# Kernel tuning notes

Hardware: AMD Instinct MI355X
Metric: run time of the kernel (lower is better)

## Reference

```python
import jax, jax.numpy as jnp
import numpy as np

N, B, S, A, H, E = 8, 8192, 64, 16, 512, 4  # agents, batch, state, action, hidden, heads
D = H // E  # attend_dim


def setup_inputs() -> dict:
    key = jax.random.key(0)
    ks = jax.random.split(key, 12)
    g = lambda k, shape, fan: (jax.random.normal(k, shape, jnp.float32) / np.float32(np.sqrt(fan)))
    return {
        "states": jax.random.normal(ks[0], (N, B, S), jnp.float32),
        "actions": jax.random.normal(ks[1], (N, B, A), jnp.float32),
        # per-agent state encoder (Linear + LeakyReLU)
        "Ws": g(ks[2], (N, S, H), S), "bs": jnp.zeros((N, H), jnp.float32),
        # per-agent state-action encoder
        "Wsa": g(ks[3], (N, S + A, H), S + A), "bsa": jnp.zeros((N, H), jnp.float32),
        # shared per-head extractors (key/selector bias-free, value has bias+LeakyReLU)
        "Wk": g(ks[4], (E, H, D), H),
        "Wsel": g(ks[5], (E, H, D), H),
        "Wv": g(ks[6], (E, H, D), H), "bv": jnp.zeros((E, D), jnp.float32),
        # per-agent critic head (2H -> H -> 1)
        "Wc1": g(ks[7], (N, 2 * H, H), 2 * H), "bc1": jnp.zeros((N, H), jnp.float32),
        "Wc2": g(ks[8], (N, H, 1), H), "bc2": jnp.zeros((N, 1), jnp.float32),
        # per-agent value head (2H -> H -> 1)
        "Wv1": g(ks[9], (N, 2 * H, H), 2 * H), "bv1": jnp.zeros((N, H), jnp.float32),
        "Wv2": g(ks[10], (N, H, 1), H), "bv2": jnp.zeros((N, 1), jnp.float32),
    }


def reference(states, actions, Ws, bs, Wsa, bsa, Wk, Wsel, Wv, bv,
              Wc1, bc1, Wc2, bc2, Wv1, bv1, Wv2, bv2):
    lrelu = jax.nn.leaky_relu  # slope 0.01, matches nn.LeakyReLU default
    # encoders: [N,B,H]
    s_enc = lrelu(jnp.einsum('nbs,nsh->nbh', states, Ws) + bs[:, None, :])
    sa = jnp.concatenate([states, actions], axis=-1)
    sa_enc = lrelu(jnp.einsum('nbi,nih->nbh', sa, Wsa) + bsa[:, None, :])
    # per-head keys/selectors/values: [B,E,N,D]
    keys = jnp.einsum('nbh,ehd->bend', sa_enc, Wk)
    sels = jnp.einsum('nbh,ehd->bend', sa_enc, Wsel)
    vals = lrelu(jnp.einsum('nbh,ehd->bend', sa_enc, Wv) + bv[None, :, None, :])
    # each agent i attends over all agents j (including itself; no mask in source)
    logits = jnp.einsum('beid,bejd->beij', sels, keys) / jnp.float32(np.sqrt(D))
    weights = jax.nn.softmax(logits, axis=-1)
    other = jnp.einsum('beij,bejd->beid', weights, vals)  # [B,E,N,D]
    other = jnp.transpose(other, (2, 0, 1, 3)).reshape(N, B, H)  # heads concat -> [N,B,H]
    critic_in = jnp.concatenate([sa_enc, other], axis=-1)  # [N,B,2H]
    value_in = jnp.concatenate([s_enc, other], axis=-1)
    q = jnp.einsum('nbh,nho->nbo', lrelu(jnp.einsum('nbi,nih->nbh', critic_in, Wc1) + bc1[:, None, :]), Wc2) + bc2[:, None, :]
    v = jnp.einsum('nbh,nho->nbo', lrelu(jnp.einsum('nbi,nih->nbh', value_in, Wv1) + bv1[:, None, :]), Wv2) + bv2[:, None, :]
    return q, v  # each [N,B,1]
```

## Files before the change

### kernel.cpp

```cpp
#include <hip/hip_runtime.h>


#define DEVI __device__ __forceinline__

typedef unsigned short us16;
typedef __bf16 bf16x8 __attribute__((ext_vector_type(8)));
typedef float f32x4 __attribute__((ext_vector_type(4)));
typedef unsigned short u16x8 __attribute__((ext_vector_type(8)));

DEVI us16 f2bf(float f) {
  unsigned u = __builtin_bit_cast(unsigned, f);
  u += 0x7FFFu + ((u >> 16) & 1u);
  return (us16)(u >> 16);
}
DEVI float bf2f(us16 h) {
  unsigned u = ((unsigned)h) << 16;
  return __builtin_bit_cast(float, u);
}
DEVI float lrelu(float v) { return v > 0.f ? v : 0.01f * v; }
DEVI int pk2(float a, float b) { return (int)f2bf(a) | ((int)f2bf(b) << 16); }

DEVI void gload16(const us16* g, us16* l) {
  __builtin_amdgcn_global_load_lds(
      (const __attribute__((address_space(1))) void*)g,
      (__attribute__((address_space(3))) void*)l, 16, 0, 0);
}

__global__ void tconvSA_k(const float* __restrict__ wsrc, const float* __restrict__ wsasrc,
                          us16* __restrict__ wst, us16* __restrict__ wsat)
{
  __shared__ float t[32][33];
  const int zz = blockIdx.z;
  const int m = zz >> 3, s = zz & 7;
  const int K = m ? 80 : 64, Kpad = m ? 96 : 64;
  const float* src = m ? (wsasrc + (long)s * 80 * 512) : (wsrc + (long)s * 64 * 512);
  us16* dst = m ? (wsat + (long)s * 512 * 96) : (wst + (long)s * 512 * 64);
  const int k0 = blockIdx.x * 32, o0 = blockIdx.y * 32;
  const int lx = threadIdx.x, ly = threadIdx.y;
#pragma unroll
  for (int i = 0; i < 4; i++) {
    int k = k0 + ly + i * 8, o = o0 + lx;
    float v = 0.f;
    if (k < K) v = src[(long)k * 512 + o];
    t[ly + i * 8][lx] = v;
  }
  __syncthreads();
#pragma unroll
  for (int i = 0; i < 4; i++) {
    int o = o0 + ly + i * 8, k = k0 + lx;
    if (k < Kpad)
      dst[(long)o * Kpad + k] = f2bf(t[lx][ly + i * 8]);
  }
}

__global__ void tconv3_k(const float* __restrict__ wk, const float* __restrict__ wsel,
                         const float* __restrict__ wv, us16* __restrict__ dst)
{
  __shared__ float t[32][33];
  const int zz = blockIdx.z;
  const int e = zz & 3, m = zz >> 2;
  const float* src = ((m == 0) ? wk : (m == 1) ? wsel : wv) + (long)e * 512 * 128;
  us16* d = dst + (long)e * 384 * 512 + (long)(m * 128) * 512;
  const int k0 = blockIdx.x * 32, o0 = blockIdx.y * 32;
  const int lx = threadIdx.x, ly = threadIdx.y;
#pragma unroll
  for (int i = 0; i < 4; i++)
    t[ly + i * 8][lx] = src[(long)(k0 + ly + i * 8) * 128 + (o0 + lx)];
  __syncthreads();
#pragma unroll
  for (int i = 0; i < 4; i++)
    d[(long)(o0 + ly + i * 8) * 512 + (k0 + lx)] = f2bf(t[lx][ly + i * 8]);
}

__global__ void tconvC_k(const float* __restrict__ c1, const float* __restrict__ v1,
                         us16* __restrict__ dc, us16* __restrict__ dv)
{
  __shared__ float t[32][33];
  const int zz = blockIdx.z;
  const int n = zz & 7, m = zz >> 3;
  const float* src = ((m == 0) ? c1 : v1) + (long)n * 1024 * 512;
  us16* dst = ((m == 0) ? dc : dv) + (long)n * 512 * 1024;
  const int k0 = blockIdx.x * 32, o0 = blockIdx.y * 32;
  const int lx = threadIdx.x, ly = threadIdx.y;
#pragma unroll
  for (int i = 0; i < 4; i++)
    t[ly + i * 8][lx] = src[(long)(k0 + ly + i * 8) * 512 + (o0 + lx)];
  __syncthreads();
#pragma unroll
  for (int i = 0; i < 4; i++)
    dst[(long)(o0 + ly + i * 8) * 1024 + (k0 + lx)] = f2bf(t[lx][ly + i * 8]);
}

enum { ASRC_F32 = 2, ASRC_F32_CAT = 3 };

template <int ASRC, int KTOT>
__global__ __launch_bounds__(256, 4)
void enc_gemm_k(const float* __restrict__ Ap, long aSlice,
                const float* __restrict__ A2p, long a2Slice,
                const us16* __restrict__ Btp, long bSlice,
                const float* __restrict__ bias, long biasSlice,
                us16* __restrict__ outB, long outSlice, long outRow)
{
  __shared__ us16 lA[128 * 32];
  __shared__ us16 lB[128 * 32];
  const int tid = threadIdx.x;
  const int z = blockIdx.z;
  const int m0 = blockIdx.x * 128;
  const int n0 = blockIdx.y * 128;
  const int wv = tid >> 6, lane = tid & 63;
  const int wm = (wv >> 1) * 64, wn = (wv & 1) * 64;
  const int fr = lane & 15, fk = (lane >> 4) * 8;
  const int rbase = (lane >> 4) * 4;
  const int grow = tid >> 2, gcol = (tid & 3) * 8;

  f32x4 acc[4][4];
#pragma unroll
  for (int i = 0; i < 4; i++)
#pragma unroll
    for (int j = 0; j < 4; j++) acc[i][j] = f32x4{0.f, 0.f, 0.f, 0.f};

  const us16* bbase = Btp + (long)z * bSlice + (long)n0 * KTOT;

  for (int k0 = 0; k0 < KTOT; k0 += 32) {
    int4 ra0, ra1;
    {
      const int srow = tid >> 1, scol0 = (tid & 1) * 16;
      const int kg = k0 + scol0;
      const float* a = nullptr;
      if constexpr (ASRC == ASRC_F32) {
        a = Ap + (long)z * aSlice + (long)(m0 + srow) * 64 + kg;
      } else {
        if (kg < 64)      a = Ap + (long)z * aSlice + (long)(m0 + srow) * 64 + kg;
        else if (kg < 80) a = A2p + (long)z * a2Slice + (long)(m0 + srow) * 16 + (kg - 64);
      }
      float4 f0, f1, f2, f3;
      if (a) { const float4* ap = (const float4*)a; f0 = ap[0]; f1 = ap[1]; f2 = ap[2]; f3 = ap[3]; }
      else   { f0 = make_float4(0.f, 0.f, 0.f, 0.f); f1 = f0; f2 = f0; f3 = f0; }
      ra0.x = pk2(f0.x, f0.y); ra0.y = pk2(f0.z, f0.w); ra0.z = pk2(f1.x, f1.y); ra0.w = pk2(f1.z, f1.w);
      ra1.x = pk2(f2.x, f2.y); ra1.y = pk2(f2.z, f2.w); ra1.z = pk2(f3.x, f3.y); ra1.w = pk2(f3.z, f3.w);
    }

    __syncthreads();
    {
      const us16* bb = bbase + k0 + gcol;
      gload16(bb + (long)grow * KTOT, &lB[tid * 8]);
      gload16(bb + (long)(64 + grow) * KTOT, &lB[2048 + tid * 8]);
    }
    {
      const int srow = tid >> 1, scol0 = (tid & 1) * 16;
      *(int4*)&lA[srow * 32 + scol0]     = ra0;
      *(int4*)&lA[srow * 32 + scol0 + 8] = ra1;
    }
    __syncthreads();

    bf16x8 af[4], bfg[4];
#pragma unroll
    for (int f = 0; f < 4; f++) af[f]  = *(const bf16x8*)&lA[(wm + f * 16 + fr) * 32 + fk];
#pragma unroll
    for (int f = 0; f < 4; f++) bfg[f] = *(const bf16x8*)&lB[(wn + f * 16 + fr) * 32 + fk];
#pragma unroll
    for (int fm = 0; fm < 4; fm++)
#pragma unroll
      for (int fn = 0; fn < 4; fn++)
        acc[fm][fn] = __builtin_amdgcn_mfma_f32_16x16x32_bf16(af[fm], bfg[fn], acc[fm][fn], 0, 0, 0);
  }

#pragma unroll
  for (int fm = 0; fm < 4; fm++) {
#pragma unroll
    for (int fn = 0; fn < 4; fn++) {
      int col = n0 + wn + fn * 16 + fr;
      float badd = bias[(long)z * biasSlice + col];
      us16* op = outB + (long)z * outSlice + (long)(m0 + wm + fm * 16 + rbase) * outRow + col;
#pragma unroll
      for (int j = 0; j < 4; j++) {
        float v = lrelu(acc[fm][fn][j] + badd);
        op[(long)j * outRow] = f2bf(v);
      }
    }
  }
}

enum { EPI_KSV = 1, EPI_DOT = 2 };

template <bool CAT, int EPI, int KTOT>
__global__ __launch_bounds__(256, 4)
void gemm64_k(const us16* __restrict__ Ap, long aSlice,
              const us16* __restrict__ A2p, long a2Slice,
              const us16* __restrict__ Btp, long bSlice,
              const float* __restrict__ bias,
              us16* __restrict__ outB, long outSlice, long outRow,
              const float* __restrict__ dotW, float* __restrict__ partial)
{
  __shared__ us16 lA[128 * 64];
  __shared__ us16 lB[128 * 64];
  const int tid = threadIdx.x;
  const int z = blockIdx.z;
  const int m0 = blockIdx.x * 128;
  const int n0 = blockIdx.y * 128;
  const int wv = tid >> 6, lane = tid & 63;
  const int wm = (wv >> 1) * 64, wn = (wv & 1) * 64;
  const int fr = lane & 15, fk = (lane >> 4) * 8;
  const int rbase = (lane >> 4) * 4;
  const int xorkey = (fr & 7) << 3;

  f32x4 acc[4][4];
#pragma unroll
  for (int i = 0; i < 4; i++)
#pragma unroll
    for (int j = 0; j < 4; j++) acc[i][j] = f32x4{0.f, 0.f, 0.f, 0.f};

  const us16* bbase = Btp + (long)z * bSlice + (long)n0 * KTOT;

  for (int k0 = 0; k0 < KTOT; k0 += 64) {
    __syncthreads();
#pragma unroll
    for (int i = 0; i < 4; i++) {
      const int c = i * 256 + tid;
      const int r = c >> 3;
      const int col = ((c & 7) ^ (r & 7)) << 3;
      const us16* a;
      if constexpr (!CAT) {
        a = Ap + (long)z * aSlice + (long)(m0 + r) * KTOT + (k0 + col);
      } else {
        const int kg = k0 + col;
        a = (kg < 512) ? Ap  + (long)z * aSlice  + (long)(m0 + r) * 512 + kg
                       : A2p + (long)z * a2Slice + (long)(m0 + r) * 512 + (kg - 512);
      }
      gload16(a, &lA[c * 8]);
    }
#pragma unroll
    for (int i = 0; i < 4; i++) {
      const int c = i * 256 + tid;
      const int r = c >> 3;
      const int col = ((c & 7) ^ (r & 7)) << 3;
      gload16(bbase + (long)r * KTOT + (k0 + col), &lB[c * 8]);
    }
    __syncthreads();

#pragma unroll
    for (int ks = 0; ks < 2; ks++) {
      bf16x8 af[4], bfg[4];
      const int kc = ks * 32 + fk;
#pragma unroll
      for (int f = 0; f < 4; f++)
        af[f]  = *(const bf16x8*)&lA[(wm + f * 16 + fr) * 64 + (kc ^ xorkey)];
#pragma unroll
      for (int f = 0; f < 4; f++)
        bfg[f] = *(const bf16x8*)&lB[(wn + f * 16 + fr) * 64 + (kc ^ xorkey)];
#pragma unroll
      for (int fm = 0; fm < 4; fm++)
#pragma unroll
        for (int fn = 0; fn < 4; fn++)
          acc[fm][fn] = __builtin_amdgcn_mfma_f32_16x16x32_bf16(af[fm], bfg[fn], acc[fm][fn], 0, 0, 0);
    }
  }

  if constexpr (EPI == EPI_DOT) {
    const float* bsl = bias + (long)z * 512;
    const float* wsl = dotW + (long)z * 512;
#pragma unroll
    for (int fm = 0; fm < 4; fm++) {
#pragma unroll
      for (int j = 0; j < 4; j++) {
        float p = 0.f;
#pragma unroll
        for (int fn = 0; fn < 4; fn++) {
          int col = n0 + wn + fn * 16 + fr;
          float v = acc[fm][fn][j] + bsl[col];
          v = lrelu(v);
          p += v * wsl[col];
        }
        p += __shfl_xor(p, 1); p += __shfl_xor(p, 2); p += __shfl_xor(p, 4); p += __shfl_xor(p, 8);
        if (fr == 0) {
          long row = (long)z * 8192 + (m0 + wm + fm * 16 + rbase + j);
          partial[row * 8 + blockIdx.y * 2 + (wv & 1)] = p;
        }
      }
    }
  } else {
#pragma unroll
    for (int fm = 0; fm < 4; fm++) {
#pragma unroll
      for (int fn = 0; fn < 4; fn++) {
        int col = n0 + wn + fn * 16 + fr;
        float badd = 0.f; bool act = false;
        if (col >= 256) { badd = bias[col - 256]; act = true; }
        us16* op = outB + (long)z * outSlice + (long)(m0 + wm + fm * 16 + rbase) * outRow + col;
#pragma unroll
        for (int j = 0; j < 4; j++) {
          float v = acc[fm][fn][j] + badd;
          if (act) v = lrelu(v);
          op[(long)j * outRow] = f2bf(v);
        }
      }
    }
  }
}

__global__ __launch_bounds__(256, 4)
void ksv2_k(const us16* __restrict__ enc, const us16* __restrict__ wkvst2,
            const float* __restrict__ bv2h, us16* __restrict__ ksv2)
{
  __shared__ us16 lA[128 * 64];
  __shared__ us16 lB[128 * 64];
  constexpr int KTOT = 512;
  const int tid = threadIdx.x;
  const int z = blockIdx.z;
  const int el = blockIdx.y / 3;
  const int n0 = (blockIdx.y % 3) * 128;
  const int m0 = blockIdx.x * 128;
  const int wv = tid >> 6, lane = tid & 63;
  const int wm = (wv >> 1) * 64, wn = (wv & 1) * 64;
  const int fr = lane & 15, fk = (lane >> 4) * 8;
  const int rbase = (lane >> 4) * 4;
  const int xorkey = (fr & 7) << 3;

  f32x4 acc[4][4];
#pragma unroll
  for (int i = 0; i < 4; i++)
#pragma unroll
    for (int j = 0; j < 4; j++) acc[i][j] = f32x4{0.f, 0.f, 0.f, 0.f};

  const us16* abase = enc + (long)z * 8192 * 512 + (long)m0 * KTOT;
  const us16* bbase = wkvst2 + ((long)el * 384 + n0) * KTOT;

  for (int k0 = 0; k0 < KTOT; k0 += 64) {
    __syncthreads();
#pragma unroll
    for (int i = 0; i < 4; i++) {
      const int c = i * 256 + tid;
      const int r = c >> 3;
      const int col = ((c & 7) ^ (r & 7)) << 3;
      gload16(abase + (long)r * KTOT + (k0 + col), &lA[c * 8]);
    }
#pragma unroll
    for (int i = 0; i < 4; i++) {
      const int c = i * 256 + tid;
      const int r = c >> 3;
      const int col = ((c & 7) ^ (r & 7)) << 3;
      gload16(bbase + (long)r * KTOT + (k0 + col), &lB[c * 8]);
    }
    __syncthreads();

#pragma unroll
    for (int ks = 0; ks < 2; ks++) {
      bf16x8 af[4], bfg[4];
      const int kc = ks * 32 + fk;
#pragma unroll
      for (int f = 0; f < 4; f++)
        af[f]  = *(const bf16x8*)&lA[(wm + f * 16 + fr) * 64 + (kc ^ xorkey)];
#pragma unroll
      for (int f = 0; f < 4; f++)
        bfg[f] = *(const bf16x8*)&lB[(wn + f * 16 + fr) * 64 + (kc ^ xorkey)];
#pragma unroll
      for (int fm = 0; fm < 4; fm++)
#pragma unroll
        for (int fn = 0; fn < 4; fn++)
          acc[fm][fn] = __builtin_amdgcn_mfma_f32_16x16x32_bf16(af[fm], bfg[fn], acc[fm][fn], 0, 0, 0);
    }
  }

#pragma unroll
  for (int fm = 0; fm < 4; fm++) {
#pragma unroll
    for (int fn = 0; fn < 4; fn++) {
      int col = n0 + wn + fn * 16 + fr;
      float badd = 0.f; bool act = false;
      if (col >= 256) { badd = bv2h[el * 128 + (col - 256)]; act = true; }
      us16* op = ksv2 + (long)(m0 + wm + fm * 16 + rbase) * 6144 + el * 3072 + z * 384 + col;
#pragma unroll
      for (int j = 0; j < 4; j++) {
        float v = acc[fm][fn][j] + badd;
        if (act) v = lrelu(v);
        op[(long)j * 6144] = f2bf(v);
      }
    }
  }
}

__global__ __launch_bounds__(256, 4)
void ksv4_k(const us16* __restrict__ enc, const us16* __restrict__ wkvst,
            const float* __restrict__ bv, us16* __restrict__ ksv4)
{
  __shared__ us16 lA[128 * 64];
  __shared__ us16 lB[128 * 64];
  constexpr int KTOT = 512;
  const int tid = threadIdx.x;
  const int z = blockIdx.z;
  const int e = blockIdx.y / 3;
  const int n0 = (blockIdx.y % 3) * 128;
  const int m0 = blockIdx.x * 128;
  const int wv = tid >> 6, lane = tid & 63;
  const int wm = (wv >> 1) * 64, wn = (wv & 1) * 64;
  const int fr = lane & 15, fk = (lane >> 4) * 8;
  const int rbase = (lane >> 4) * 4;
  const int xorkey = (fr & 7) << 3;

  f32x4 acc[4][4];
#pragma unroll
  for (int i = 0; i < 4; i++)
#pragma unroll
    for (int j = 0; j < 4; j++) acc[i][j] = f32x4{0.f, 0.f, 0.f, 0.f};

  const us16* abase = enc + (long)z * 8192 * 512 + (long)m0 * KTOT;
  const us16* bbase = wkvst + ((long)e * 384 + n0) * KTOT;

  for (int k0 = 0; k0 < KTOT; k0 += 64) {
    __syncthreads();
#pragma unroll
    for (int i = 0; i < 4; i++) {
      const int c = i * 256 + tid;
      const int r = c >> 3;
      const int col = ((c & 7) ^ (r & 7)) << 3;
      gload16(abase + (long)r * KTOT + (k0 + col), &lA[c * 8]);
    }
#pragma unroll
    for (int i = 0; i < 4; i++) {
      const int c = i * 256 + tid;
      const int r = c >> 3;
      const int col = ((c & 7) ^ (r & 7)) << 3;
      gload16(bbase + (long)r * KTOT + (k0 + col), &lB[c * 8]);
    }
    __syncthreads();

#pragma unroll
    for (int ks = 0; ks < 2; ks++) {
      bf16x8 af[4], bfg[4];
      const int kc = ks * 32 + fk;
#pragma unroll
      for (int f = 0; f < 4; f++)
        af[f]  = *(const bf16x8*)&lA[(wm + f * 16 + fr) * 64 + (kc ^ xorkey)];
#pragma unroll
      for (int f = 0; f < 4; f++)
        bfg[f] = *(const bf16x8*)&lB[(wn + f * 16 + fr) * 64 + (kc ^ xorkey)];
#pragma unroll
      for (int fm = 0; fm < 4; fm++)
#pragma unroll
        for (int fn = 0; fn < 4; fn++)
          acc[fm][fn] = __builtin_amdgcn_mfma_f32_16x16x32_bf16(af[fm], bfg[fn], acc[fm][fn], 0, 0, 0);
    }
  }

#pragma unroll
  for (int fm = 0; fm < 4; fm++) {
#pragma unroll
    for (int fn = 0; fn < 4; fn++) {
      int col = n0 + wn + fn * 16 + fr;
      float badd = 0.f; bool act = false;
      if (col >= 256) { badd = bv[e * 128 + (col - 256)]; act = true; }
      us16* op = ksv4 + (long)(m0 + wm + fm * 16 + rbase) * 12288 + e * 3072 + z * 384 + col;
#pragma unroll
      for (int j = 0; j < 4; j++) {
        float v = acc[fm][fn][j] + badd;
        if (act) v = lrelu(v);
        op[(long)j * 12288] = f2bf(v);
      }
    }
  }
}

__global__ __launch_bounds__(256, 4)
void dot2_k(const us16* __restrict__ encC, const us16* __restrict__ encV,
            const us16* __restrict__ other,
            const us16* __restrict__ wc1t, const us16* __restrict__ wv1t,
            const float* __restrict__ bc1, const float* __restrict__ bv1,
            const float* __restrict__ wc2, const float* __restrict__ wv2,
            float* __restrict__ partial)
{
  __shared__ us16 lA[128 * 64];
  __shared__ us16 lB[128 * 64];
  constexpr int KTOT = 1024;
  const int tid = threadIdx.x;
  const int zz = blockIdx.z;
  const int half = zz >> 3, z = zz & 7;
  const us16* Ap  = half ? encV : encC;
  const us16* Btp = half ? wv1t : wc1t;
  const float* bias = half ? bv1 : bc1;
  const float* dotW = half ? wv2 : wc2;
  const int m0 = blockIdx.x * 128;
  const int n0 = blockIdx.y * 128;
  const int wv = tid >> 6, lane = tid & 63;
  const int wm = (wv >> 1) * 64, wn = (wv & 1) * 64;
  const int fr = lane & 15, fk = (lane >> 4) * 8;
  const int rbase = (lane >> 4) * 4;
  const int xorkey = (fr & 7) << 3;

  f32x4 acc[4][4];
#pragma unroll
  for (int i = 0; i < 4; i++)
#pragma unroll
    for (int j = 0; j < 4; j++) acc[i][j] = f32x4{0.f, 0.f, 0.f, 0.f};

  const us16* bbase = Btp + (long)z * 512 * 1024 + (long)n0 * KTOT;
  const long aSlice = (long)8192 * 512;

  for (int k0 = 0; k0 < KTOT; k0 += 64) {
    __syncthreads();
#pragma unroll
    for (int i = 0; i < 4; i++) {
      const int c = i * 256 + tid;
      const int r = c >> 3;
      const int col = ((c & 7) ^ (r & 7)) << 3;
      const int kg = k0 + col;
      const us16* a = (kg < 512) ? Ap    + (long)z * aSlice + (long)(m0 + r) * 512 + kg
                                 : other + (long)z * aSlice + (long)(m0 + r) * 512 + (kg - 512);
      gload16(a, &lA[c * 8]);
    }
#pragma unroll
    for (int i = 0; i < 4; i++) {
      const int c = i * 256 + tid;
      const int r = c >> 3;
      const int col = ((c & 7) ^ (r & 7)) << 3;
      gload16(bbase + (long)r * KTOT + (k0 + col), &lB[c * 8]);
    }
    __syncthreads();

#pragma unroll
    for (int ks = 0; ks < 2; ks++) {
      bf16x8 af[4], bfg[4];
      const int kc = ks * 32 + fk;
#pragma unroll
      for (int f = 0; f < 4; f++)
        af[f]  = *(const bf16x8*)&lA[(wm + f * 16 + fr) * 64 + (kc ^ xorkey)];
#pragma unroll
      for (int f = 0; f < 4; f++)
        bfg[f] = *(const bf16x8*)&lB[(wn + f * 16 + fr) * 64 + (kc ^ xorkey)];
#pragma unroll
      for (int fm = 0; fm < 4; fm++)
#pragma unroll
        for (int fn = 0; fn < 4; fn++)
          acc[fm][fn] = __builtin_amdgcn_mfma_f32_16x16x32_bf16(af[fm], bfg[fn], acc[fm][fn], 0, 0, 0);
    }
  }

  const float* bsl = bias + (long)z * 512;
  const float* wsl = dotW + (long)z * 512;
#pragma unroll
  for (int fm = 0; fm < 4; fm++) {
#pragma unroll
    for (int j = 0; j < 4; j++) {
      float p = 0.f;
#pragma unroll
      for (int fn = 0; fn < 4; fn++) {
        int col = n0 + wn + fn * 16 + fr;
        float v = acc[fm][fn][j] + bsl[col];
        v = lrelu(v);
        p += v * wsl[col];
      }
      p += __shfl_xor(p, 1); p += __shfl_xor(p, 2); p += __shfl_xor(p, 4); p += __shfl_xor(p, 8);
      if (fr == 0) {
        long row = (long)half * 65536 + (long)z * 8192 + (m0 + wm + fm * 16 + rbase + j);
        partial[row * 8 + blockIdx.y * 2 + (wv & 1)] = p;
      }
    }
  }
}

DEVI void attn_core(const us16* __restrict__ src, us16* __restrict__ other,
                    int e, long b, int lane, us16* tbuf)
{
#pragma unroll
  for (int i = 0; i < 6; i++) {
    int c = i * 64 + lane;
    int r = c / 48, cc = c - r * 48;
    *(int4*)&tbuf[r * 392 + cc * 8] = *(const int4*)&src[c * 8];
  }
  __syncthreads();
  const int i = lane >> 3, j = lane & 7;
  const us16* selp = &tbuf[i * 392 + 128];
  const us16* keyp = &tbuf[j * 392];
  float acc = 0.f;
#pragma unroll
  for (int d = 0; d < 128; d += 8) {
    u16x8 s8 = *(const u16x8*)&selp[d];
    u16x8 k8 = *(const u16x8*)&keyp[d];
#pragma unroll
    for (int q = 0; q < 8; q++) acc += bf2f(s8[q]) * bf2f(k8[q]);
  }
  acc *= 0.088388347648318447f;
  float mx = acc;
  mx = fmaxf(mx, __shfl_xor(mx, 1)); mx = fmaxf(mx, __shfl_xor(mx, 2)); mx = fmaxf(mx, __shfl_xor(mx, 4));
  float ex = __expf(acc - mx);
  float sm = ex;
  sm += __shfl_xor(sm, 1); sm += __shfl_xor(sm, 2); sm += __shfl_xor(sm, 4);
  float wsm = ex / sm;
  float wj[8];
  const int ibase = lane & 56;
#pragma unroll
  for (int jj = 0; jj < 8; jj++) wj[jj] = __shfl(wsm, ibase + jj);
  const int dbase = (lane & 7) * 16;
  float o[16];
#pragma unroll
  for (int q = 0; q < 16; q++) o[q] = 0.f;
#pragma unroll
  for (int jj = 0; jj < 8; jj++) {
    u16x8 v0 = *(const u16x8*)&tbuf[jj * 392 + 256 + dbase];
    u16x8 v1 = *(const u16x8*)&tbuf[jj * 392 + 256 + dbase + 8];
    float wgt = wj[jj];
#pragma unroll
    for (int q = 0; q < 8; q++) { o[q] += wgt * bf2f(v0[q]); o[8 + q] += wgt * bf2f(v1[q]); }
  }
  u16x8 r0, r1;
#pragma unroll
  for (int q = 0; q < 8; q++) { r0[q] = f2bf(o[q]); r1[q] = f2bf(o[8 + q]); }
  us16* dst = other + ((long)i * 8192 + b) * 512 + e * 128 + dbase;
  *(u16x8*)&dst[0] = r0;
  *(u16x8*)&dst[8] = r1;
}

__global__ __launch_bounds__(256, 4)
void attn_k(const us16* __restrict__ ksv, us16* __restrict__ other, int e)
{
  __shared__ us16 t[4][8 * 392];
  const int wv = threadIdx.x >> 6, lane = threadIdx.x & 63;
  const long b = (long)blockIdx.x * 4 + wv;
  attn_core(ksv + b * 3072, other, e, b, lane, &t[wv][0]);
}

__global__ __launch_bounds__(256, 4)
void attn2_k(const us16* __restrict__ ksv2, us16* __restrict__ other, int ebase)
{
  __shared__ us16 t[4][8 * 392];
  const int wv = threadIdx.x >> 6, lane = threadIdx.x & 63;
  const long b = (long)blockIdx.x * 4 + wv;
  const int el = blockIdx.y;
  attn_core(ksv2 + b * 6144 + el * 3072, other, ebase + el, b, lane, &t[wv][0]);
}

__global__ __launch_bounds__(256, 4)
void attn4_k(const us16* __restrict__ ksv4, us16* __restrict__ other)
{
  __shared__ us16 t[4][8 * 392];
  const int wv = threadIdx.x >> 6, lane = threadIdx.x & 63;
  const long b = (long)blockIdx.x * 4 + wv;
  const int e = blockIdx.y;
  attn_core(ksv4 + b * 12288 + e * 3072, other, e, b, lane, &t[wv][0]);
}

__global__ void reduce2_k(const float* __restrict__ part, const float* __restrict__ b2c,
                          const float* __restrict__ b2v, float* __restrict__ out)
{
  int r = blockIdx.x * 256 + threadIdx.x;
  const float4* p = (const float4*)(part + (long)r * 8);
  float4 a = p[0], b = p[1];
  float s = ((a.x + a.y) + (a.z + a.w)) + ((b.x + b.y) + (b.z + b.w));
  int agent = (r >> 13) & 7;
  out[r] = s + ((r < 65536) ? b2c[agent] : b2v[agent]);
}

extern "C" void kernel_launch(void* const* d_in, const int* in_sizes, int n_in,
                              void* d_out, int out_size, void* d_ws, size_t ws_size,
                              hipStream_t stream)
{
  const float* states = (const float*)d_in[0];
  const float* actions= (const float*)d_in[1];
  const float* Ws  = (const float*)d_in[2];
  const float* bs  = (const float*)d_in[3];
  const float* Wsa = (const float*)d_in[4];
  const float* bsa = (const float*)d_in[5];
  const float* Wk  = (const float*)d_in[6];
  const float* Wsel= (const float*)d_in[7];
  const float* Wv  = (const float*)d_in[8];
  const float* bv  = (const float*)d_in[9];
  const float* Wc1 = (const float*)d_in[10];
  const float* bc1 = (const float*)d_in[11];
  const float* Wc2 = (const float*)d_in[12];
  const float* bc2 = (const float*)d_in[13];
  const float* Wv1 = (const float*)d_in[14];
  const float* bv1 = (const float*)d_in[15];
  const float* Wv2 = (const float*)d_in[16];
  const float* bv2 = (const float*)d_in[17];

  char* ws = (char*)d_ws;
  constexpr size_t OFF_WST   = 0;
  constexpr size_t OFF_WSAT  = OFF_WST   + (size_t)8 * 512 * 64 * 2;
  constexpr size_t OFF_WKVST = OFF_WSAT  + (size_t)8 * 512 * 96 * 2;
  constexpr size_t OFF_WC1T  = OFF_WKVST + (size_t)4 * 384 * 512 * 2;
  constexpr size_t OFF_WV1T  = OFF_WC1T  + (size_t)8 * 512 * 1024 * 2;
  constexpr size_t OFF_ENC   = OFF_WV1T  + (size_t)8 * 512 * 1024 * 2;
  constexpr size_t OFF_OTHER = OFF_ENC   + (size_t)8 * 8192 * 512 * 2;
  constexpr size_t OFF_KSV   = OFF_OTHER + (size_t)8 * 8192 * 512 * 2;
  constexpr size_t OFF_PARTB = OFF_KSV   + (size_t)8192 * 8 * 384 * 2;
  constexpr size_t NEED_B    = OFF_PARTB + (size_t)131072 * 8 * 4;
  constexpr size_t KSV2_BYTES = (size_t)8192 * 2 * 8 * 384 * 2;
  constexpr size_t NEED_A2    = OFF_KSV + KSV2_BYTES;
  constexpr size_t KSV4_BYTES = (size_t)8192 * 4 * 8 * 384 * 2;
  constexpr size_t NEED_A4    = OFF_KSV + KSV4_BYTES;
  constexpr size_t OFF_PARTA  = OFF_KSV;
  constexpr size_t OFF_ENC2   = OFF_KSV + (size_t)131072 * 8 * 4;
  if (ws_size < NEED_B) return;
  const int tier = (ws_size >= NEED_A4) ? 2 : (ws_size >= NEED_A2) ? 1 : 0;

  us16* WST   = (us16*)(ws + OFF_WST);
  us16* WSAT  = (us16*)(ws + OFF_WSAT);
  us16* WKVST = (us16*)(ws + OFF_WKVST);
  us16* WC1T  = (us16*)(ws + OFF_WC1T);
  us16* WV1T  = (us16*)(ws + OFF_WV1T);
  us16* ENC   = (us16*)(ws + OFF_ENC);
  us16* OTHER = (us16*)(ws + OFF_OTHER);
  us16* KSV   = (us16*)(ws + OFF_KSV);
  float* PARTB= (float*)(ws + OFF_PARTB);
  float* PARTA= (float*)(ws + OFF_PARTA);
  us16* ENC2  = (us16*)(ws + OFF_ENC2);

  dim3 tb(32, 8);
  tconvSA_k<<<dim3(3, 16, 16), tb, 0, stream>>>(Ws, Wsa, WST, WSAT);
  tconv3_k <<<dim3(16, 4, 12), tb, 0, stream>>>(Wk, Wsel, Wv, WKVST);
  tconvC_k <<<dim3(32, 16, 16),tb, 0, stream>>>(Wc1, Wv1, WC1T, WV1T);

  enc_gemm_k<ASRC_F32_CAT, 96><<<dim3(64, 4, 8), 256, 0, stream>>>(
      states, (long)8192 * 64, actions, (long)8192 * 16, WSAT, (long)512 * 96, bsa, 512,
      ENC, (long)8192 * 512, 512);

  if (tier == 2) {
    ksv4_k<<<dim3(64, 12, 8), 256, 0, stream>>>(ENC, WKVST, bv, KSV);
    attn4_k<<<dim3(2048, 4), 256, 0, stream>>>(KSV, OTHER);
    enc_gemm_k<ASRC_F32, 64><<<dim3(64, 4, 8), 256, 0, stream>>>(
        states, (long)8192 * 64, nullptr, 0, WST, (long)512 * 64, bs, 512,
        ENC2, (long)8192 * 512, 512);
    dot2_k<<<dim3(64, 4, 16), 256, 0, stream>>>(
        ENC, ENC2, OTHER, WC1T, WV1T, bc1, bv1, Wc2, Wv2, PARTA);
    reduce2_k<<<dim3(512), 256, 0, stream>>>(PARTA, bc2, bv2, (float*)d_out);
  } else if (tier == 1) {
    for (int h = 0; h < 2; h++) {
      ksv2_k<<<dim3(64, 6, 8), 256, 0, stream>>>(
          ENC, WKVST + (size_t)(h * 2) * 384 * 512, bv + h * 256, KSV);
      attn2_k<<<dim3(2048, 2), 256, 0, stream>>>(KSV, OTHER, h * 2);
    }
    enc_gemm_k<ASRC_F32, 64><<<dim3(64, 4, 8), 256, 0, stream>>>(
        states, (long)8192 * 64, nullptr, 0, WST, (long)512 * 64, bs, 512,
        ENC2, (long)8192 * 512, 512);
    dot2_k<<<dim3(64, 4, 16), 256, 0, stream>>>(
        ENC, ENC2, OTHER, WC1T, WV1T, bc1, bv1, Wc2, Wv2, PARTA);
    reduce2_k<<<dim3(512), 256, 0, stream>>>(PARTA, bc2, bv2, (float*)d_out);
  } else {
    for (int e = 0; e < 4; e++) {
      gemm64_k<false, EPI_KSV, 512><<<dim3(64, 3, 8), 256, 0, stream>>>(
          ENC, (long)8192 * 512, nullptr, 0, WKVST + (size_t)e * 384 * 512, 0, bv + e * 128,
          KSV, 384, 3072, nullptr, nullptr);
      attn_k<<<dim3(2048), 256, 0, stream>>>(KSV, OTHER, e);
    }
    gemm64_k<true, EPI_DOT, 1024><<<dim3(64, 4, 8), 256, 0, stream>>>(
        ENC, (long)8192 * 512, OTHER, (long)8192 * 512, WC1T, (long)512 * 1024, bc1,
        nullptr, 0, 0, Wc2, PARTB);
    enc_gemm_k<ASRC_F32, 64><<<dim3(64, 4, 8), 256, 0, stream>>>(
        states, (long)8192 * 64, nullptr, 0, WST, (long)512 * 64, bs, 512,
        ENC, (long)8192 * 512, 512);
    gemm64_k<true, EPI_DOT, 1024><<<dim3(64, 4, 8), 256, 0, stream>>>(
        ENC, (long)8192 * 512, OTHER, (long)8192 * 512, WV1T, (long)512 * 1024, bv1,
        nullptr, 0, 0, Wv2, PARTB + (size_t)65536 * 8);
    reduce2_k<<<dim3(512), 256, 0, stream>>>(PARTB, bc2, bv2, (float*)d_out);
  }
}
```

Measured before the change: 393.1 us.

## Add triple-buffered 256x128 tile critic/value GEMM with 512-thread blocks

```diff
diff --git a/kernel.cpp b/kernel.cpp
--- a/kernel.cpp
+++ b/kernel.cpp
@@ -557,6 +557,128 @@
   }
 }
 
+__global__ __launch_bounds__(512, 1)
+void dotP_k(const us16* __restrict__ encC, const us16* __restrict__ encV,
+            const us16* __restrict__ other,
+            const us16* __restrict__ wc1t, const us16* __restrict__ wv1t,
+            const float* __restrict__ bc1, const float* __restrict__ bv1,
+            const float* __restrict__ wc2, const float* __restrict__ wv2,
+            float* __restrict__ partial)
+{
+  extern __shared__ us16 lds[];
+  constexpr int KTOT = 1024;
+  const int tid = threadIdx.x;
+  const int zz = blockIdx.z;
+  const int half = zz >> 3, z = zz & 7;
+  const us16* Ap  = half ? encV : encC;
+  const us16* Btp = half ? wv1t : wc1t;
+  const float* bias = half ? bv1 : bc1;
+  const float* dotW = half ? wv2 : wc2;
+  const int m0 = blockIdx.x * 256;
+  const int n0 = blockIdx.y * 128;
+  const int wv = tid >> 6, lane = tid & 63;
+  const int wr = wv >> 2, wc = wv & 3;
+  const int wmBase = wr * 128, wnBase = wc * 32;
+  const int fr = lane & 15, fk = (lane >> 4) * 8;
+  const int rbase = (lane >> 4) * 4;
+  const int srow = tid >> 3;
+  const int scol = ((tid & 7) ^ (srow & 7)) << 3;
+  const long aSlice = (long)8192 * 512;
+  const us16* bb = Btp + (long)z * 512 * 1024 + (long)n0 * KTOT;
+
+  f32x4 acc[8][2];
+#pragma unroll
+  for (int i = 0; i < 8; i++)
+#pragma unroll
+    for (int j = 0; j < 2; j++) acc[i][j] = f32x4{0.f, 0.f, 0.f, 0.f};
+
+  auto stage = [&](int t, int buf) {
+    us16* base = lds + buf * 24576;
+    const int k0 = t * 64;
+    const int kg = k0 + scol;
+#pragma unroll
+    for (int g = 0; g < 4; g++) {
+      const int r = g * 64 + srow;
+      const us16* a = (kg < 512) ? Ap    + (long)z * aSlice + (long)(m0 + r) * 512 + kg
+                                 : other + (long)z * aSlice + (long)(m0 + r) * 512 + (kg - 512);
+      gload16(a, base + g * 4096 + tid * 8);
+    }
+#pragma unroll
+    for (int g = 0; g < 2; g++) {
+      const int r = g * 64 + srow;
+      gload16(bb + (long)r * KTOT + (k0 + scol), base + 16384 + g * 4096 + tid * 8);
+    }
+  };
+
+  constexpr int NT = KTOT / 64;
+  stage(0, 0);
+  stage(1, 1);
+
+  int cur = 0;
+#pragma unroll 1
+  for (int t = 0; t < NT; ++t) {
+    if (t + 1 < NT) asm volatile("s_waitcnt vmcnt(6)" ::: "memory");
+    else            asm volatile("s_waitcnt vmcnt(0)" ::: "memory");
+    __builtin_amdgcn_sched_barrier(0);
+    __builtin_amdgcn_s_barrier();
+    __builtin_amdgcn_sched_barrier(0);
+
+    const int nxt2 = (cur >= 1) ? cur - 1 : cur + 2;
+    if (t + 2 < NT) stage(t + 2, nxt2);
+
+    const us16* curA = lds + cur * 24576;
+    const us16* curB = curA + 16384;
+
+    bf16x8 bfg[2][2];
+#pragma unroll
+    for (int fn = 0; fn < 2; fn++)
+#pragma unroll
+      for (int ks = 0; ks < 2; ks++) {
+        const int row = wnBase + fn * 16 + fr;
+        bfg[fn][ks] = *(const bf16x8*)&curB[row * 64 + ((ks * 32 + fk) ^ ((row & 7) << 3))];
+      }
+    __builtin_amdgcn_s_setprio(1);
+#pragma unroll
+    for (int fm = 0; fm < 8; fm++) {
+      bf16x8 af0, af1;
+      const int row = wmBase + fm * 16 + fr;
+      af0 = *(const bf16x8*)&curA[row * 64 + ((fk) ^ ((row & 7) << 3))];
+      af1 = *(const bf16x8*)&curA[row * 64 + ((32 + fk) ^ ((row & 7) << 3))];
+#pragma unroll
+      for (int fn = 0; fn < 2; fn++) {
+        acc[fm][fn] = __builtin_amdgcn_mfma_f32_16x16x32_bf16(af0, bfg[fn][0], acc[fm][fn], 0, 0, 0);
+        acc[fm][fn] = __builtin_amdgcn_mfma_f32_16x16x32_bf16(af1, bfg[fn][1], acc[fm][fn], 0, 0, 0);
+      }
+    }
+    __builtin_amdgcn_s_setprio(0);
+    __builtin_amdgcn_s_barrier();
+    __builtin_amdgcn_sched_barrier(0);
+    cur = (cur + 1 < 3) ? cur + 1 : 0;
+  }
+
+  const float* bsl = bias + (long)z * 512;
+  const float* wsl = dotW + (long)z * 512;
+#pragma unroll
+  for (int fm = 0; fm < 8; fm++) {
+#pragma unroll
+    for (int j = 0; j < 4; j++) {
+      float p = 0.f;
+#pragma unroll
+      for (int fn = 0; fn < 2; fn++) {
+        int col = n0 + wnBase + fn * 16 + fr;
+        float v = acc[fm][fn][j] + bsl[col];
+        v = lrelu(v);
+        p += v * wsl[col];
+      }
+      p += __shfl_xor(p, 1); p += __shfl_xor(p, 2); p += __shfl_xor(p, 4); p += __shfl_xor(p, 8);
+      if (fr == 0) {
+        long row = (long)half * 65536 + (long)z * 8192 + (m0 + wmBase + fm * 16 + rbase + j);
+        partial[row * 16 + blockIdx.y * 4 + wc] = p;
+      }
+    }
+  }
+}
+
 DEVI void attn_core(const us16* __restrict__ src, us16* __restrict__ other,
                     int e, long b, int lane, us16* tbuf)
 {
@@ -645,6 +767,21 @@
   const float4* p = (const float4*)(part + (long)r * 8);
   float4 a = p[0], b = p[1];
   float s = ((a.x + a.y) + (a.z + a.w)) + ((b.x + b.y) + (b.z + b.w));
+  int agent = (r >> 13) & 7;
+  out[r] = s + ((r < 65536) ? b2c[agent] : b2v[agent]);
+}
+
+__global__ void reduce16_k(const float* __restrict__ part, const float* __restrict__ b2c,
+                           const float* __restrict__ b2v, float* __restrict__ out)
+{
+  int r = blockIdx.x * 256 + threadIdx.x;
+  const float4* p = (const float4*)(part + (long)r * 16);
+  float s = 0.f;
+#pragma unroll
+  for (int i = 0; i < 4; i++) {
+    float4 a = p[i];
+    s += ((a.x + a.y) + (a.z + a.w));
+  }
   int agent = (r >> 13) & 7;
   out[r] = s + ((r < 65536) ? b2c[agent] : b2v[agent]);
 }
@@ -688,7 +825,8 @@
   constexpr size_t KSV4_BYTES = (size_t)8192 * 4 * 8 * 384 * 2;
   constexpr size_t NEED_A4    = OFF_KSV + KSV4_BYTES;
   constexpr size_t OFF_PARTA  = OFF_KSV;
-  constexpr size_t OFF_ENC2   = OFF_KSV + (size_t)131072 * 8 * 4;
+  constexpr size_t OFF_ENC2_8 = OFF_KSV + (size_t)131072 * 8 * 4;
+  constexpr size_t OFF_ENC2_16= OFF_KSV + (size_t)131072 * 16 * 4;
   if (ws_size < NEED_B) return;
   const int tier = (ws_size >= NEED_A4) ? 2 : (ws_size >= NEED_A2) ? 1 : 0;
 
@@ -702,7 +840,11 @@
   us16* KSV   = (us16*)(ws + OFF_KSV);
   float* PARTB= (float*)(ws + OFF_PARTB);
   float* PARTA= (float*)(ws + OFF_PARTA);
-  us16* ENC2  = (us16*)(ws + OFF_ENC2);
+
+  const bool pipeOK =
+      hipFuncSetAttribute((const void*)dotP_k,
+                          hipFuncAttributeMaxDynamicSharedMemorySize, 147456) == hipSuccess;
+  us16* ENC2 = (us16*)(ws + (pipeOK ? OFF_ENC2_16 : OFF_ENC2_8));
 
   dim3 tb(32, 8);
   tconvSA_k<<<dim3(3, 16, 16), tb, 0, stream>>>(Ws, Wsa, WST, WSAT);
@@ -719,20 +861,27 @@
     enc_gemm_k<ASRC_F32, 64><<<dim3(64, 4, 8), 256, 0, stream>>>(
         states, (long)8192 * 64, nullptr, 0, WST, (long)512 * 64, bs, 512,
         ENC2, (long)8192 * 512, 512);
-    dot2_k<<<dim3(64, 4, 16), 256, 0, stream>>>(
-        ENC, ENC2, OTHER, WC1T, WV1T, bc1, bv1, Wc2, Wv2, PARTA);
-    reduce2_k<<<dim3(512), 256, 0, stream>>>(PARTA, bc2, bv2, (float*)d_out);
+    if (pipeOK) {
+      dotP_k<<<dim3(32, 4, 16), 512, 147456, stream>>>(
+          ENC, ENC2, OTHER, WC1T, WV1T, bc1, bv1, Wc2, Wv2, PARTA);
+      reduce16_k<<<dim3(512), 256, 0, stream>>>(PARTA, bc2, bv2, (float*)d_out);
+    } else {
+      dot2_k<<<dim3(64, 4, 16), 256, 0, stream>>>(
+          ENC, ENC2, OTHER, WC1T, WV1T, bc1, bv1, Wc2, Wv2, PARTA);
+      reduce2_k<<<dim3(512), 256, 0, stream>>>(PARTA, bc2, bv2, (float*)d_out);
+    }
   } else if (tier == 1) {
     for (int h = 0; h < 2; h++) {
       ksv2_k<<<dim3(64, 6, 8), 256, 0, stream>>>(
           ENC, WKVST + (size_t)(h * 2) * 384 * 512, bv + h * 256, KSV);
       attn2_k<<<dim3(2048, 2), 256, 0, stream>>>(KSV, OTHER, h * 2);
     }
+    us16* ENC2b = (us16*)(ws + OFF_ENC2_8);
     enc_gemm_k<ASRC_F32, 64><<<dim3(64, 4, 8), 256, 0, stream>>>(
         states, (long)8192 * 64, nullptr, 0, WST, (long)512 * 64, bs, 512,
-        ENC2, (long)8192 * 512, 512);
+        ENC2b, (long)8192 * 512, 512);
     dot2_k<<<dim3(64, 4, 16), 256, 0, stream>>>(
-        ENC, ENC2, OTHER, WC1T, WV1T, bc1, bv1, Wc2, Wv2, PARTA);
+        ENC, ENC2b, OTHER, WC1T, WV1T, bc1, bv1, Wc2, Wv2, PARTA);
     reduce2_k<<<dim3(512), 256, 0, stream>>>(PARTA, bc2, bv2, (float*)d_out);
   } else {
     for (int e = 0; e < 4; e++) {
```

Result: no change. 393.5 us (+0.1%).
